# Optimization experiments

Measured on AMD Instinct MI355X. Metric: run time of the kernel, lower is better.

Reference implementation:

```python
import jax, jax.numpy as jnp
import numpy as np

BSZ, N_VARS, IN_DIM, OUT_DIM, N_CLUSTER = 128, 321, 336, 96, 8


def setup_inputs() -> dict:
    key = jax.random.key(0)
    k1, k2, k3, k4 = jax.random.split(key, 4)
    x = jax.random.normal(k1, (BSZ, N_VARS, IN_DIM), dtype=jnp.float32)
    prob = jax.random.uniform(k2, (BSZ, N_VARS, N_CLUSTER), dtype=jnp.float32)
    # per-cluster Linear params, stacked: W[c] is (out_dim, in_dim), b[c] is (out_dim,)
    bound = 1.0 / np.sqrt(IN_DIM)
    W = jax.random.uniform(k3, (N_CLUSTER, OUT_DIM, IN_DIM), minval=-bound, maxval=bound, dtype=jnp.float32)
    b = jax.random.uniform(k4, (N_CLUSTER, OUT_DIM), minval=-bound, maxval=bound, dtype=jnp.float32)
    return {"x": x, "prob": prob, "W": W, "b": b}


def reference(x, prob, W, b):
    # Original: for each cluster c, y_c = x @ W[c].T + b[c]  -> stack (b,v,out,c)
    # then matmul with prob (b,v,c,1) -> prob-weighted combine over clusters.
    # Fused: combine cluster weighting inline, never materializing the stack.
    # x: (b, v, i); W: (c, o, i); prob: (b, v, c) -> out: (b, v, o)
    out = jnp.einsum('bvi,coi,bvc->bvo', x, W, prob)
    out = out + jnp.einsum('bvc,co->bvo', prob, b)
    return out
```

## Files before the change

### kernel.cpp

```cpp
#include <hip/hip_runtime.h>

#define BSZ 128
#define NV 321
#define IN_DIM 336
#define OUT_DIM 96
#define NC 8
#define ROWS (BSZ * NV)
#define KP 352
#define LDK 360
#define KSTEPS 11

typedef _Float16 half8 __attribute__((ext_vector_type(8)));
typedef _Float16 half4 __attribute__((ext_vector_type(4)));
typedef float floatx4 __attribute__((ext_vector_type(4)));

__global__ __launch_bounds__(256) void convert_w_kernel(
    const float* __restrict__ W, const float* __restrict__ b,
    _Float16* __restrict__ w16) {
  int idx = blockIdx.x * 256 + threadIdx.x;
  if (idx >= NC * OUT_DIM * KP) return;
  int row = idx / KP;
  int k = idx - row * KP;
  float v;
  if (k < IN_DIM)       v = W[row * IN_DIM + k];
  else if (k == IN_DIM) v = b[row];
  else                  v = 0.0f;
  w16[idx] = (_Float16)v;
}

__global__ __launch_bounds__(256) void cluster_gemm_kernel(
    const float* __restrict__ x, const float* __restrict__ prob,
    const _Float16* __restrict__ w16, float* __restrict__ out) {
  __shared__ _Float16 xs[64 * LDK];

  const int tid = threadIdx.x;
  const int rbase = blockIdx.x * 64;

  {
    int row = tid >> 2;
    int q = tid & 3;
    const float* src = x + (size_t)(rbase + row) * IN_DIM + q * 84;
    _Float16* dst = xs + row * LDK + q * 84;
#pragma unroll
    for (int j = 0; j < 21; ++j) {
      floatx4 v = *(const floatx4*)(src + j * 4);
      half4 h = {(_Float16)v[0], (_Float16)v[1], (_Float16)v[2], (_Float16)v[3]};
      *(half4*)(dst + j * 4) = h;
    }
    if (tid < 64) {
      _Float16* p = xs + tid * LDK + IN_DIM;
      p[0] = (_Float16)1.0f;
#pragma unroll
      for (int k = 1; k < LDK - IN_DIM; ++k) p[k] = (_Float16)0.0f;
    }
  }
  __syncthreads();

  const int lane = tid & 63;
  const int wave = tid >> 6;
  const int wm = wave >> 1;
  const int wc = wave & 1;
  const int l15 = lane & 15;
  const int lg = lane >> 4;

  const _Float16* a_base = xs + (wm * 32 + l15) * LDK + lg * 8;

  const _Float16* bp0 = w16 + (size_t)(wc * 48 + 0 * 16 + l15) * KP + lg * 8;
  const _Float16* bp1 = w16 + (size_t)(wc * 48 + 1 * 16 + l15) * KP + lg * 8;
  const _Float16* bp2 = w16 + (size_t)(wc * 48 + 2 * 16 + l15) * KP + lg * 8;

  floatx4 oacc[2][3] = {};

  for (int c = 0; c < NC; ++c) {
    floatx4 acc[2][3] = {};
    const size_t coff = (size_t)c * OUT_DIM * KP;
#pragma unroll
    for (int ks = 0; ks < KSTEPS; ++ks) {
      half8 a0 = *(const half8*)(a_base + ks * 32);
      half8 a1 = *(const half8*)(a_base + 16 * LDK + ks * 32);
      half8 b0 = *(const half8*)(bp0 + coff + ks * 32);
      half8 b1 = *(const half8*)(bp1 + coff + ks * 32);
      half8 b2 = *(const half8*)(bp2 + coff + ks * 32);
      acc[0][0] = __builtin_amdgcn_mfma_f32_16x16x32_f16(a0, b0, acc[0][0], 0, 0, 0);
      acc[1][0] = __builtin_amdgcn_mfma_f32_16x16x32_f16(a1, b0, acc[1][0], 0, 0, 0);
      acc[0][1] = __builtin_amdgcn_mfma_f32_16x16x32_f16(a0, b1, acc[0][1], 0, 0, 0);
      acc[1][1] = __builtin_amdgcn_mfma_f32_16x16x32_f16(a1, b1, acc[1][1], 0, 0, 0);
      acc[0][2] = __builtin_amdgcn_mfma_f32_16x16x32_f16(a0, b2, acc[0][2], 0, 0, 0);
      acc[1][2] = __builtin_amdgcn_mfma_f32_16x16x32_f16(a1, b2, acc[1][2], 0, 0, 0);
    }
#pragma unroll
    for (int m = 0; m < 2; ++m) {
#pragma unroll
      for (int r = 0; r < 4; ++r) {
        float p = prob[(size_t)(rbase + wm * 32 + m * 16 + lg * 4 + r) * NC + c];
        oacc[m][0][r] += p * acc[m][0][r];
        oacc[m][1][r] += p * acc[m][1][r];
        oacc[m][2][r] += p * acc[m][2][r];
      }
    }
  }

#pragma unroll
  for (int m = 0; m < 2; ++m) {
#pragma unroll
    for (int n = 0; n < 3; ++n) {
#pragma unroll
      for (int r = 0; r < 4; ++r) {
        int grow = rbase + wm * 32 + m * 16 + lg * 4 + r;
        out[(size_t)grow * OUT_DIM + wc * 48 + n * 16 + l15] = oacc[m][n][r];
      }
    }
  }
}

extern "C" void kernel_launch(void* const* d_in, const int* in_sizes, int n_in,
                              void* d_out, int out_size, void* d_ws, size_t ws_size,
                              hipStream_t stream) {
  const float* x = (const float*)d_in[0];
  const float* prob = (const float*)d_in[1];
  const float* W = (const float*)d_in[2];
  const float* b = (const float*)d_in[3];
  float* out = (float*)d_out;
  _Float16* w16 = (_Float16*)d_ws;

  const int wtotal = NC * OUT_DIM * KP;
  hipLaunchKernelGGL(convert_w_kernel, dim3((wtotal + 255) / 256), dim3(256), 0,
                     stream, W, b, w16);
  hipLaunchKernelGGL(cluster_gemm_kernel, dim3(ROWS / 64), dim3(256), 0, stream,
                     x, prob, w16, out);
}
```

Before: 149.2 us.

## Keep x tile in registers and stream packed weight chunks via LDS ring

The x tile now goes straight from global memory into half8 registers, with the bias column folded in as a one, instead of being staged in LDS. Weights are repacked into contiguous 32-wide K chunks. Those chunks are streamed into a 6-deep LDS ring with global_load_lds, gated by vmcnt waits and barriers, and B fragments are prefetched one step ahead. Prob values are cached in LDS. This hides weight fetch latency and avoids redundant global weight reads per wave, at the cost of high register pressure from 22 resident A fragments and a barrier on every K step.

```diff
diff --git a/kernel.cpp b/kernel.cpp
--- a/kernel.cpp
+++ b/kernel.cpp
@@ -6,56 +6,73 @@
 #define OUT_DIM 96
 #define NC 8
 #define ROWS (BSZ * NV)
-#define KP 352
-#define LDK 360
 #define KSTEPS 11
+#define NCH (NC * KSTEPS)
+#define CHUNK_HALFS 3072
+#define CHUNK_BYTES 6144
+#define NRING 6
 
 typedef _Float16 half8 __attribute__((ext_vector_type(8)));
-typedef _Float16 half4 __attribute__((ext_vector_type(4)));
 typedef float floatx4 __attribute__((ext_vector_type(4)));
+typedef float floatx2 __attribute__((ext_vector_type(2)));
 
 __global__ __launch_bounds__(256) void convert_w_kernel(
     const float* __restrict__ W, const float* __restrict__ b,
-    _Float16* __restrict__ w16) {
-  int idx = blockIdx.x * 256 + threadIdx.x;
-  if (idx >= NC * OUT_DIM * KP) return;
-  int row = idx / KP;
-  int k = idx - row * KP;
-  float v;
-  if (k < IN_DIM)       v = W[row * IN_DIM + k];
-  else if (k == IN_DIM) v = b[row];
-  else                  v = 0.0f;
-  w16[idx] = (_Float16)v;
-}
-
-__global__ __launch_bounds__(256) void cluster_gemm_kernel(
+    _Float16* __restrict__ w16p) {
+  int t = blockIdx.x * 256 + threadIdx.x;
+  if (t >= NC * KSTEPS * OUT_DIM * 4) return;
+  int kk0 = (t & 3) * 8;
+  int o = (t >> 2) % OUT_DIM;
+  int chunk = (t >> 2) / OUT_DIM;
+  int ks = chunk % KSTEPS;
+  int c = chunk / KSTEPS;
+  int k0 = ks * 32 + kk0;
+  const float* wr = W + (size_t)(c * OUT_DIM + o) * IN_DIM;
+  half8 h;
+#pragma unroll
+  for (int j = 0; j < 8; ++j) {
+    int k = k0 + j;
+    float v = (k < IN_DIM) ? wr[k] : ((k == IN_DIM) ? b[c * OUT_DIM + o] : 0.0f);
+    h[j] = (_Float16)v;
+  }
+  *(half8*)(w16p + (size_t)chunk * CHUNK_HALFS + o * 32 + kk0) = h;
+}
+
+__device__ __forceinline__ void stage16(const _Float16* g, const _Float16* l) {
+  __builtin_amdgcn_global_load_lds(
+      (const __attribute__((address_space(1))) void*)g,
+      (__attribute__((address_space(3))) void*)l, 16, 0, 0);
+}
+
+__device__ __forceinline__ void vm_wait(int n) {
+  if (n <= 0)      asm volatile("s_waitcnt vmcnt(0)" ::: "memory");
+  else if (n == 1) asm volatile("s_waitcnt vmcnt(1)" ::: "memory");
+  else if (n == 2) asm volatile("s_waitcnt vmcnt(2)" ::: "memory");
+  else if (n == 3) asm volatile("s_waitcnt vmcnt(3)" ::: "memory");
+  else if (n == 4) asm volatile("s_waitcnt vmcnt(4)" ::: "memory");
+  else if (n == 5) asm volatile("s_waitcnt vmcnt(5)" ::: "memory");
+  else if (n == 6) asm volatile("s_waitcnt vmcnt(6)" ::: "memory");
+  else if (n == 7) asm volatile("s_waitcnt vmcnt(7)" ::: "memory");
+  else             asm volatile("s_waitcnt vmcnt(8)" ::: "memory");
+}
+
+__device__ __forceinline__ half8 cvt8(floatx4 f0, floatx4 f1) {
+  half8 h;
+  h[0] = (_Float16)f0[0]; h[1] = (_Float16)f0[1];
+  h[2] = (_Float16)f0[2]; h[3] = (_Float16)f0[3];
+  h[4] = (_Float16)f1[0]; h[5] = (_Float16)f1[1];
+  h[6] = (_Float16)f1[2]; h[7] = (_Float16)f1[3];
+  return h;
+}
+
+__global__ __launch_bounds__(256, 2) void cluster_gemm_kernel(
     const float* __restrict__ x, const float* __restrict__ prob,
-    const _Float16* __restrict__ w16, float* __restrict__ out) {
-  __shared__ _Float16 xs[64 * LDK];
+    const _Float16* __restrict__ w16p, float* __restrict__ out) {
+  __shared__ __align__(16) _Float16 bb[NRING][CHUNK_HALFS];
+  __shared__ float probs[64 * NC];
 
   const int tid = threadIdx.x;
   const int rbase = blockIdx.x * 64;
-
-  {
-    int row = tid >> 2;
-    int q = tid & 3;
-    const float* src = x + (size_t)(rbase + row) * IN_DIM + q * 84;
-    _Float16* dst = xs + row * LDK + q * 84;
-#pragma unroll
-    for (int j = 0; j < 21; ++j) {
-      floatx4 v = *(const floatx4*)(src + j * 4);
-      half4 h = {(_Float16)v[0], (_Float16)v[1], (_Float16)v[2], (_Float16)v[3]};
-      *(half4*)(dst + j * 4) = h;
-    }
-    if (tid < 64) {
-      _Float16* p = xs + tid * LDK + IN_DIM;
-      p[0] = (_Float16)1.0f;
-#pragma unroll
-      for (int k = 1; k < LDK - IN_DIM; ++k) p[k] = (_Float16)0.0f;
-    }
-  }
-  __syncthreads();
-
   const int lane = tid & 63;
   const int wave = tid >> 6;
   const int wm = wave >> 1;
@@ -63,41 +80,114 @@
   const int l15 = lane & 15;
   const int lg = lane >> 4;
 
-  const _Float16* a_base = xs + (wm * 32 + l15) * LDK + lg * 8;
-
-  const _Float16* bp0 = w16 + (size_t)(wc * 48 + 0 * 16 + l15) * KP + lg * 8;
-  const _Float16* bp1 = w16 + (size_t)(wc * 48 + 1 * 16 + l15) * KP + lg * 8;
-  const _Float16* bp2 = w16 + (size_t)(wc * 48 + 2 * 16 + l15) * KP + lg * 8;
+  {
+    floatx2 v = *(const floatx2*)(prob + (size_t)rbase * NC + tid * 2);
+    *(floatx2*)&probs[tid * 2] = v;
+  }
+
+  half8 a[2][KSTEPS];
+#pragma unroll
+  for (int m = 0; m < 2; ++m) {
+    const float* xr = x + (size_t)(rbase + wm * 32 + m * 16 + l15) * IN_DIM + lg * 8;
+#pragma unroll
+    for (int ks = 0; ks < 10; ++ks) {
+      floatx4 f0 = *(const floatx4*)(xr + ks * 32);
+      floatx4 f1 = *(const floatx4*)(xr + ks * 32 + 4);
+      a[m][ks] = cvt8(f0, f1);
+    }
+    if (lg < 2) {
+      floatx4 f0 = *(const floatx4*)(xr + 320);
+      floatx4 f1 = *(const floatx4*)(xr + 320 + 4);
+      a[m][10] = cvt8(f0, f1);
+    } else {
+      half8 z = {};
+      if (lg == 2) z[0] = (_Float16)1.0f;
+      a[m][10] = z;
+    }
+  }
+
+  asm volatile("s_waitcnt vmcnt(0)" ::: "memory");
+
+  const int seg0 = (wave < 2) ? wave * 2048 : 4096 + (wave - 2) * 1024;
+  const int nseg = (wave < 2) ? 2 : 1;
+  const int lane16 = lane * 16;
+
+#define STAGE(CH)                                                              \
+  do {                                                                         \
+    const _Float16* gsrc =                                                     \
+        w16p + (size_t)(CH)*CHUNK_HALFS;                                       \
+    stage16((const _Float16*)((const char*)gsrc + seg0 + lane16),              \
+            (const _Float16*)((const char*)&bb[(CH) % NRING][0] + seg0));      \
+    if (nseg == 2)                                                             \
+      stage16((const _Float16*)((const char*)gsrc + seg0 + 1024 + lane16),     \
+              (const _Float16*)((const char*)&bb[(CH) % NRING][0] + seg0 +     \
+                               1024));                                         \
+  } while (0)
+
+  STAGE(0); STAGE(1); STAGE(2); STAGE(3); STAGE(4);
+
+  if (wave < 2) vm_wait(8); else vm_wait(4);
+  asm volatile("s_waitcnt lgkmcnt(0)" ::: "memory");
+  __builtin_amdgcn_s_barrier();
+
+  const int rdoff = (wc * 48 + l15) * 32 + lg * 8;
+
+  half8 bcur0 = *(const half8*)(&bb[0][rdoff]);
+  half8 bcur1 = *(const half8*)(&bb[0][rdoff + 512]);
+  half8 bcur2 = *(const half8*)(&bb[0][rdoff + 1024]);
 
   floatx4 oacc[2][3] = {};
-
-  for (int c = 0; c < NC; ++c) {
-    floatx4 acc[2][3] = {};
-    const size_t coff = (size_t)c * OUT_DIM * KP;
-#pragma unroll
-    for (int ks = 0; ks < KSTEPS; ++ks) {
-      half8 a0 = *(const half8*)(a_base + ks * 32);
-      half8 a1 = *(const half8*)(a_base + 16 * LDK + ks * 32);
-      half8 b0 = *(const half8*)(bp0 + coff + ks * 32);
-      half8 b1 = *(const half8*)(bp1 + coff + ks * 32);
-      half8 b2 = *(const half8*)(bp2 + coff + ks * 32);
-      acc[0][0] = __builtin_amdgcn_mfma_f32_16x16x32_f16(a0, b0, acc[0][0], 0, 0, 0);
-      acc[1][0] = __builtin_amdgcn_mfma_f32_16x16x32_f16(a1, b0, acc[1][0], 0, 0, 0);
-      acc[0][1] = __builtin_amdgcn_mfma_f32_16x16x32_f16(a0, b1, acc[0][1], 0, 0, 0);
-      acc[1][1] = __builtin_amdgcn_mfma_f32_16x16x32_f16(a1, b1, acc[1][1], 0, 0, 0);
-      acc[0][2] = __builtin_amdgcn_mfma_f32_16x16x32_f16(a0, b2, acc[0][2], 0, 0, 0);
-      acc[1][2] = __builtin_amdgcn_mfma_f32_16x16x32_f16(a1, b2, acc[1][2], 0, 0, 0);
-    }
-#pragma unroll
-    for (int m = 0; m < 2; ++m) {
-#pragma unroll
-      for (int r = 0; r < 4; ++r) {
-        float p = prob[(size_t)(rbase + wm * 32 + m * 16 + lg * 4 + r) * NC + c];
-        oacc[m][0][r] += p * acc[m][0][r];
-        oacc[m][1][r] += p * acc[m][1][r];
-        oacc[m][2][r] += p * acc[m][2][r];
+  floatx4 acc[2][3] = {};
+
+#pragma unroll
+  for (int it = 0; it < NCH; ++it) {
+    const int c = it / KSTEPS;
+    const int ks = it % KSTEPS;
+
+    {
+      int rem = 86 - it; if (rem < 0) rem = 0;
+      const int base = rem > 3 ? 3 : rem;
+      if (wave < 2) vm_wait(base * 2); else vm_wait(base);
+    }
+    __builtin_amdgcn_s_barrier();
+
+    if (it + 5 < NCH) STAGE(it + 5);
+
+    half8 bn0, bn1, bn2;
+    if (it + 1 < NCH) {
+      const _Float16* bp = &bb[(it + 1) % NRING][rdoff];
+      bn0 = *(const half8*)(bp);
+      bn1 = *(const half8*)(bp + 512);
+      bn2 = *(const half8*)(bp + 1024);
+    }
+
+    acc[0][0] = __builtin_amdgcn_mfma_f32_16x16x32_f16(a[0][ks], bcur0, acc[0][0], 0, 0, 0);
+    acc[1][0] = __builtin_amdgcn_mfma_f32_16x16x32_f16(a[1][ks], bcur0, acc[1][0], 0, 0, 0);
+    acc[0][1] = __builtin_amdgcn_mfma_f32_16x16x32_f16(a[0][ks], bcur1, acc[0][1], 0, 0, 0);
+    acc[1][1] = __builtin_amdgcn_mfma_f32_16x16x32_f16(a[1][ks], bcur1, acc[1][1], 0, 0, 0);
+    acc[0][2] = __builtin_amdgcn_mfma_f32_16x16x32_f16(a[0][ks], bcur2, acc[0][2], 0, 0, 0);
+    acc[1][2] = __builtin_amdgcn_mfma_f32_16x16x32_f16(a[1][ks], bcur2, acc[1][2], 0, 0, 0);
+
+    if (ks == KSTEPS - 1) {
+#pragma unroll
+      for (int m = 0; m < 2; ++m) {
+#pragma unroll
+        for (int r = 0; r < 4; ++r) {
+          float p = probs[(wm * 32 + m * 16 + lg * 4 + r) * NC + c];
+          oacc[m][0][r] += p * acc[m][0][r];
+          oacc[m][1][r] += p * acc[m][1][r];
+          oacc[m][2][r] += p * acc[m][2][r];
+        }
       }
-    }
+#pragma unroll
+      for (int m = 0; m < 2; ++m) {
+        acc[m][0] = (floatx4){0.f, 0.f, 0.f, 0.f};
+        acc[m][1] = (floatx4){0.f, 0.f, 0.f, 0.f};
+        acc[m][2] = (floatx4){0.f, 0.f, 0.f, 0.f};
+      }
+    }
+
+    bcur0 = bn0; bcur1 = bn1; bcur2 = bn2;
   }
 
 #pragma unroll
@@ -111,6 +201,7 @@
       }
     }
   }
+#undef STAGE
 }
 
 extern "C" void kernel_launch(void* const* d_in, const int* in_sizes, int n_in,
@@ -121,11 +212,11 @@
   const float* W = (const float*)d_in[2];
   const float* b = (const float*)d_in[3];
   float* out = (float*)d_out;
-  _Float16* w16 = (_Float16*)d_ws;
-
-  const int wtotal = NC * OUT_DIM * KP;
-  hipLaunchKernelGGL(convert_w_kernel, dim3((wtotal + 255) / 256), dim3(256), 0,
-                     stream, W, b, w16);
+  _Float16* w16p = (_Float16*)d_ws;
+
+  const int ct = NC * KSTEPS * OUT_DIM * 4;
+  hipLaunchKernelGGL(convert_w_kernel, dim3((ct + 255) / 256), dim3(256), 0,
+                     stream, W, b, w16p);
   hipLaunchKernelGGL(cluster_gemm_kernel, dim3(ROWS / 64), dim3(256), 0, stream,
-                     x, prob, w16, out);
-}
+                     x, prob, w16p, out);
+}
```

Result: slower. 176.0 us (+17.9%).
